# Kernel optimization log

Hardware: AMD Instinct MI355X
Metric: run time of the kernel (lower is better)

## Reference

```python
import jax, jax.numpy as jnp
import numpy as np

D_STATE = 8
DT_RANK = 8  # ceil(128/16)


def _grouped_1x1(x, w):
    # x: (B,H,W,Cin), w: (g, Cout//g, Cin//g)
    B, H, W, _ = x.shape
    g, o, i = w.shape
    xg = x.reshape(B, H, W, g, i)
    return jnp.einsum('bhwgi,goi->bhwgo', xg, w).reshape(B, H, W, g * o)


def setup_inputs() -> dict:
    key = jax.random.key(0)
    ks = jax.random.split(key, 16)
    B, H, W, C = 8, 64, 64, 128
    g = 4
    D = 128  # expand_dim = d_inner
    N = D_STATE
    R = DT_RANK
    inp = {}
    inp['x'] = jax.random.normal(ks[0], (B, H, W, C), dtype=jnp.float32)
    inp['w1'] = jax.random.normal(ks[1], (g, D // g, C // g), dtype=jnp.float32) * 0.1
    inp['dw'] = jax.random.normal(ks[2], (3, 3, 1, D), dtype=jnp.float32) * 0.1  # HWIO depthwise
    inp['in_proj_w'] = jax.random.normal(ks[3], (2 * D, D), dtype=jnp.float32) * 0.05
    inp['conv1d_w'] = jax.random.normal(ks[4], (D, 3), dtype=jnp.float32) * 0.1
    inp['conv1d_b'] = jax.random.normal(ks[5], (D,), dtype=jnp.float32) * 0.05
    inp['x_proj_w'] = jax.random.normal(ks[6], (R + 2 * N, D), dtype=jnp.float32) * 0.05
    inp['dt_proj_w'] = jax.random.normal(ks[7], (D, R), dtype=jnp.float32) * 0.05
    inp['dt_proj_b'] = jax.random.normal(ks[8], (D,), dtype=jnp.float32) * 0.05
    inp['A_log'] = jnp.log(jnp.tile(jnp.arange(1, N + 1, dtype=jnp.float32)[None, :], (D, 1)))
    inp['D_param'] = jnp.ones((D,), dtype=jnp.float32)
    inp['out_proj_w'] = jax.random.normal(ks[9], (D, D), dtype=jnp.float32) * 0.05
    inp['gamma'] = jnp.ones((D,), dtype=jnp.float32)
    inp['beta'] = jnp.zeros((D,), dtype=jnp.float32)
    inp['w2'] = jax.random.normal(ks[10], (g, D // g, C // g), dtype=jnp.float32) * 0.1
    inp['wout'] = jax.random.normal(ks[11], (g, C // g, D // g), dtype=jnp.float32) * 0.1
    return inp


def _mamba(x_seq, in_proj_w, conv1d_w, conv1d_b, x_proj_w, dt_proj_w, dt_proj_b, A_log, D_param, out_proj_w):
    # x_seq: (B, L, D)
    B, L, D = x_seq.shape
    N, R = D_STATE, DT_RANK
    xz = jnp.einsum('bld,ed->ble', x_seq, in_proj_w)  # (B,L,2D)
    u, z = xz[..., :D], xz[..., D:]
    # causal depthwise conv1d, kernel=3, left pad 2 (torch: padding=2, slice [:L])
    up = jnp.pad(u, ((0, 0), (2, 0), (0, 0)))
    u = (up[:, 0:L] * conv1d_w[:, 0] + up[:, 1:L + 1] * conv1d_w[:, 1]
         + up[:, 2:L + 2] * conv1d_w[:, 2] + conv1d_b)
    u = jax.nn.silu(u)
    x_dbl = jnp.einsum('bld,ed->ble', u, x_proj_w)  # (B,L,R+2N)
    dt = x_dbl[..., :R]
    Bm = x_dbl[..., R:R + N]
    Cm = x_dbl[..., R + N:]
    delta = jax.nn.softplus(jnp.einsum('blr,dr->bld', dt, dt_proj_w) + dt_proj_b)  # (B,L,D)
    A = -jnp.exp(A_log)  # (D,N)

    def step(h, inp):
        d_t, u_t, b_t, c_t = inp  # (B,D),(B,D),(B,N),(B,N)
        dA = jnp.exp(d_t[..., None] * A)            # (B,D,N)
        h = dA * h + (d_t * u_t)[..., None] * b_t[:, None, :]
        y_t = jnp.einsum('bdn,bn->bd', h, c_t)
        return h, y_t

    h0 = jnp.zeros((B, D, N), dtype=x_seq.dtype)
    xs = (jnp.swapaxes(delta, 0, 1), jnp.swapaxes(u, 0, 1),
          jnp.swapaxes(Bm, 0, 1), jnp.swapaxes(Cm, 0, 1))
    _, ys = jax.lax.scan(step, h0, xs)              # ys: (L,B,D)
    y = jnp.swapaxes(ys, 0, 1) + u * D_param
    y = y * jax.nn.silu(z)
    return jnp.einsum('bld,ed->ble', y, out_proj_w)


def reference(x, w1, dw, in_proj_w, conv1d_w, conv1d_b, x_proj_w, dt_proj_w, dt_proj_b,
              A_log, D_param, out_proj_w, gamma, beta, w2, wout):
    B, H, W, C = x.shape
    D = dw.shape[-1]
    x1 = _grouped_1x1(x, w1)  # (B,H,W,D)
    x1 = jax.lax.conv_general_dilated(
        x1, dw, window_strides=(1, 1), padding='SAME',
        feature_group_count=D, dimension_numbers=('NHWC', 'HWIO', 'NHWC'))
    x1 = jax.nn.silu(x1)
    x1_seq = x1.reshape(B, H * W, D)
    x1_seq = _mamba(x1_seq, in_proj_w, conv1d_w, conv1d_b, x_proj_w,
                    dt_proj_w, dt_proj_b, A_log, D_param, out_proj_w)
    x1 = x1_seq.reshape(B, H, W, D)
    mu = jnp.mean(x1, axis=-1, keepdims=True)
    var = jnp.mean(jnp.square(x1 - mu), axis=-1, keepdims=True)
    x1 = (x1 - mu) * jax.lax.rsqrt(var + 1e-5) * gamma + beta
    x2 = jax.nn.silu(_grouped_1x1(x, w2))
    x_fuse = x1 * x2
    return _grouped_1x1(x_fuse, wout)  # (B,H,W,C)
```

## Files before the change

### kernel.cpp

```cpp
#include <hip/hip_runtime.h>
#include <math.h>

#define B_    8
#define C_    128
#define D_    128
#define L_    4096
#define NPOS_ 32768
#define NC_   256
#define S_    16
#define MFL_  1048576

typedef __attribute__((ext_vector_type(8))) short short8;
typedef __attribute__((ext_vector_type(4))) float f32x4;

__device__ __forceinline__ float siluf(float x) { return x / (1.f + __expf(-x)); }
__device__ __forceinline__ float softplusf(float x) {
    if (x > 20.f) return x;
    return __logf(1.f + __expf(x));
}
__device__ __forceinline__ unsigned short f2bf(float f) {
    unsigned int u = __float_as_uint(f);
    u = (u + 0x7FFFu + ((u >> 16) & 1u)) >> 16;
    return (unsigned short)u;
}
__device__ __forceinline__ float bf2f(unsigned short h) {
    return __uint_as_float(((unsigned int)h) << 16);
}
__device__ __forceinline__ void scan_as(float dl, const float* Ar, bool fast, float* a) {
    if (fast) {
        float e1 = __expf(-dl);
        a[0] = e1;
        a[1] = e1 * e1;
        a[2] = a[1] * e1;
        a[3] = a[1] * a[1];
        a[4] = a[3] * e1;
        a[5] = a[3] * a[1];
        a[6] = a[5] * e1;
        a[7] = a[3] * a[3];
    } else {
        #pragma unroll
        for (int n = 0; n < 8; ++n) a[n] = __expf(dl * Ar[n]);
    }
}

__global__ __launch_bounds__(256) void k0_cvt(const float* __restrict__ inW,
                                              const float* __restrict__ OW,
                                              const float* __restrict__ xpw,
                                              unsigned short* __restrict__ inWb,
                                              unsigned short* __restrict__ OWb,
                                              unsigned short* __restrict__ xpwb) {
    for (int i = blockIdx.x * 256 + threadIdx.x; i < 52224; i += gridDim.x * 256) {
        if (i < 32768)      inWb[i] = f2bf(inW[i]);
        else if (i < 49152) OWb[i - 32768] = f2bf(OW[i - 32768]);
        else                xpwb[i - 49152] = f2bf(xpw[i - 49152]);
    }
}

__global__ __launch_bounds__(256) void k1_g1x1(const float* __restrict__ x,
                                               const float* __restrict__ w1,
                                               const float* __restrict__ w2,
                                               unsigned short* __restrict__ t1b,
                                               unsigned short* __restrict__ x2sb) {
    __shared__ float xs[16 * 128];
    int t = threadIdx.x;
    int d = t & 127, ph = t >> 7;
    int g = d >> 5, o = d & 31;
    float w1r[32], w2r[32];
    #pragma unroll
    for (int i = 0; i < 32; ++i) {
        w1r[i] = w1[g * 1024 + o * 32 + i];
        w2r[i] = w2[g * 1024 + o * 32 + i];
    }
    int pos0 = blockIdx.x * 64;
    for (int it = 0; it < 4; ++it) {
        int p0 = pos0 + it * 16;
        #pragma unroll
        for (int q = 0; q < 2; ++q) {
            int fi = t * 2 + q;
            *(float4*)&xs[fi * 4] = *(const float4*)&x[p0 * 128 + fi * 4];
        }
        __syncthreads();
        #pragma unroll
        for (int q = 0; q < 8; ++q) {
            int pl = ph * 8 + q;
            float a1 = 0.f, a2 = 0.f;
            const float* xr = &xs[pl * 128 + g * 32];
            #pragma unroll
            for (int i4 = 0; i4 < 8; ++i4) {
                float4 xv = *(const float4*)&xr[i4 * 4];
                a1 += xv.x * w1r[i4*4] + xv.y * w1r[i4*4+1] + xv.z * w1r[i4*4+2] + xv.w * w1r[i4*4+3];
                a2 += xv.x * w2r[i4*4] + xv.y * w2r[i4*4+1] + xv.z * w2r[i4*4+2] + xv.w * w2r[i4*4+3];
            }
            int pos = p0 + pl;
            t1b[pos * 128 + d]  = f2bf(a1);
            x2sb[pos * 128 + d] = f2bf(siluf(a2));
        }
        __syncthreads();
    }
}

__global__ __launch_bounds__(128) void k2_dwconv(const unsigned short* __restrict__ t1b,
                                                 const float* __restrict__ dw,
                                                 unsigned short* __restrict__ x1cb) {
    int d = threadIdx.x;
    float dwr[9];
    #pragma unroll
    for (int k = 0; k < 9; ++k) dwr[k] = dw[k * 128 + d];
    int bid = blockIdx.x;
    int wt = bid & 7, ht = (bid >> 3) & 7, b = bid >> 6;
    int h0 = ht * 8, w0 = wt * 8;
    float rows[10][10];
    #pragma unroll
    for (int r = 0; r < 10; ++r) {
        int hh = h0 - 1 + r;
        bool hv = (hh >= 0) && (hh < 64);
        #pragma unroll
        for (int c = 0; c < 10; ++c) {
            int w = w0 - 1 + c;
            bool wvv = (w >= 0) && (w < 64);
            rows[r][c] = (hv && wvv) ? bf2f(t1b[((b * 64 + hh) * 64 + w) * 128 + d]) : 0.f;
        }
    }
    #pragma unroll
    for (int hi = 0; hi < 8; ++hi) {
        #pragma unroll
        for (int wi = 0; wi < 8; ++wi) {
            float acc = rows[hi][wi]     * dwr[0] + rows[hi][wi+1]   * dwr[1] + rows[hi][wi+2]   * dwr[2]
                      + rows[hi+1][wi]   * dwr[3] + rows[hi+1][wi+1] * dwr[4] + rows[hi+1][wi+2] * dwr[5]
                      + rows[hi+2][wi]   * dwr[6] + rows[hi+2][wi+1] * dwr[7] + rows[hi+2][wi+2] * dwr[8];
            x1cb[((b * 64 + h0 + hi) * 64 + w0 + wi) * 128 + d] = f2bf(siluf(acc));
        }
    }
}

__global__ __launch_bounds__(256) void k3_mfma(const unsigned short* __restrict__ Abf,
                                               const unsigned short* __restrict__ Bbf,
                                               unsigned short* __restrict__ urawb,
                                               unsigned short* __restrict__ zb) {
    __shared__ unsigned short Al[128 * 72];
    __shared__ unsigned short Bl[128 * 72];
    int t = threadIdx.x;
    int mtile = blockIdx.x >> 1, ntile = blockIdx.x & 1;
    int pos0 = mtile * 128, n0g = ntile * 128;
    int lane = t & 63, wv = t >> 6;
    int m0 = (wv & 1) * 64, n0w = (wv >> 1) * 64;
    int lanem = lane & 15, laneq = lane >> 4;
    f32x4 acc[4][4];
    #pragma unroll
    for (int i = 0; i < 4; ++i)
        #pragma unroll
        for (int j = 0; j < 4; ++j) acc[i][j] = (f32x4){0.f, 0.f, 0.f, 0.f};
    for (int kc = 0; kc < 2; ++kc) {
        #pragma unroll
        for (int q = 0; q < 4; ++q) {
            int c = t + q * 256;
            int row = c >> 3, col = c & 7;
            *(int4*)&Al[row * 72 + col * 8] = *(const int4*)&Abf[(pos0 + row) * 128 + kc * 64 + col * 8];
            *(int4*)&Bl[row * 72 + col * 8] = *(const int4*)&Bbf[(n0g + row) * 128 + kc * 64 + col * 8];
        }
        __syncthreads();
        #pragma unroll
        for (int ks = 0; ks < 2; ++ks) {
            short8 af[4], bfr[4];
            #pragma unroll
            for (int mi = 0; mi < 4; ++mi)
                af[mi] = *(const short8*)&Al[(m0 + mi * 16 + lanem) * 72 + ks * 32 + laneq * 8];
            #pragma unroll
            for (int ni = 0; ni < 4; ++ni)
                bfr[ni] = *(const short8*)&Bl[(n0w + ni * 16 + lanem) * 72 + ks * 32 + laneq * 8];
            #pragma unroll
            for (int mi = 0; mi < 4; ++mi)
                #pragma unroll
                for (int ni = 0; ni < 4; ++ni)
                    acc[mi][ni] = __builtin_amdgcn_mfma_f32_16x16x32_bf16(af[mi], bfr[ni], acc[mi][ni], 0, 0, 0);
        }
        __syncthreads();
    }
    unsigned short* dst = ntile ? zb : urawb;
    #pragma unroll
    for (int mi = 0; mi < 4; ++mi)
        #pragma unroll
        for (int ni = 0; ni < 4; ++ni)
            #pragma unroll
            for (int r = 0; r < 4; ++r) {
                int m = pos0 + m0 + mi * 16 + laneq * 4 + r;
                int n = n0w + ni * 16 + lanem;
                dst[m * 128 + n] = f2bf(acc[mi][ni][r]);
            }
}

__global__ __launch_bounds__(256) void k4_convproj(const unsigned short* __restrict__ urawb,
                                                   const float* __restrict__ cw,
                                                   const float* __restrict__ cb,
                                                   const unsigned short* __restrict__ xpwb,
                                                   const float* __restrict__ dtw,
                                                   const float* __restrict__ dtb,
                                                   unsigned short* __restrict__ usb,
                                                   float* __restrict__ delta,
                                                   float* __restrict__ Bm,
                                                   float* __restrict__ Cm) {
    __shared__ unsigned short uA[64 * 136];
    __shared__ unsigned short xB[32 * 136];
    __shared__ float xdb[64 * 36];
    int t = threadIdx.x;
    int d = t & 127, ph = t >> 7;
    for (int i = t; i < 32 * 128; i += 256) {
        int n = i >> 7, k = i & 127;
        xB[n * 136 + k] = (n < 24) ? xpwb[n * 128 + k] : (unsigned short)0;
    }
    float cw0 = cw[d * 3 + 0], cw1 = cw[d * 3 + 1], cw2 = cw[d * 3 + 2], cbr = cb[d];
    float dtwr[8];
    #pragma unroll
    for (int r = 0; r < 8; ++r) dtwr[r] = dtw[d * 8 + r];
    float dtbr = dtb[d];

    int gpos0 = blockIdx.x * 64;
    int ll0 = (gpos0 & 4095) + ph * 32;
    int base = (gpos0 + ph * 32) * 128 + d;
    float ur0 = (ll0 >= 2) ? bf2f(urawb[base - 256]) : 0.f;
    float ur1 = (ll0 >= 1) ? bf2f(urawb[base - 128]) : 0.f;
    #pragma unroll
    for (int q = 0; q < 32; ++q) {
        float urq = bf2f(urawb[base + q * 128]);
        float v = siluf(ur0 * cw0 + ur1 * cw1 + urq * cw2 + cbr);
        unsigned short vb = f2bf(v);
        usb[base + q * 128] = vb;
        uA[(ph * 32 + q) * 136 + d] = vb;
        ur0 = ur1; ur1 = urq;
    }
    __syncthreads();
    int lane = t & 63, wv = t >> 6;
    int lanem = lane & 15, laneq = lane >> 4;
    f32x4 accx[2];
    accx[0] = (f32x4){0.f, 0.f, 0.f, 0.f};
    accx[1] = (f32x4){0.f, 0.f, 0.f, 0.f};
    #pragma unroll
    for (int ks = 0; ks < 4; ++ks) {
        short8 af = *(const short8*)&uA[(wv * 16 + lanem) * 136 + ks * 32 + laneq * 8];
        #pragma unroll
        for (int nj = 0; nj < 2; ++nj) {
            short8 bfr = *(const short8*)&xB[(nj * 16 + lanem) * 136 + ks * 32 + laneq * 8];
            accx[nj] = __builtin_amdgcn_mfma_f32_16x16x32_bf16(af, bfr, accx[nj], 0, 0, 0);
        }
    }
    #pragma unroll
    for (int nj = 0; nj < 2; ++nj)
        #pragma unroll
        for (int r = 0; r < 4; ++r)
            xdb[(wv * 16 + laneq * 4 + r) * 36 + nj * 16 + lanem] = accx[nj][r];
    __syncthreads();
    #pragma unroll
    for (int q = 0; q < 32; ++q) {
        int pl = ph * 32 + q;
        float dt = dtbr;
        #pragma unroll
        for (int r = 0; r < 8; ++r) dt += xdb[pl * 36 + r] * dtwr[r];
        delta[base + q * 128] = softplusf(dt);
    }
    for (int i = t; i < 1024; i += 256) {
        int p = i >> 4, j = i & 15;
        float v = xdb[p * 36 + 8 + j];
        int gp = gpos0 + p;
        if (j < 8) Bm[gp * 8 + j] = v;
        else       Cm[gp * 8 + (j - 8)] = v;
    }
}

__global__ __launch_bounds__(128) void k5_scan1(const float* __restrict__ delta,
                                                const unsigned short* __restrict__ usb,
                                                const float* __restrict__ Bm,
                                                const float* __restrict__ A_log,
                                                float* __restrict__ cA,
                                                float* __restrict__ cB) {
    int d = threadIdx.x;
    int bc = blockIdx.x;
    int b = bc >> 8, c = bc & 255;
    float Ar[8]; bool fast = true;
    #pragma unroll
    for (int n = 0; n < 8; ++n) {
        Ar[n] = -__expf(A_log[d * 8 + n]);
        fast = fast && (fabsf(Ar[n] + (float)(n + 1)) < 2e-3f);
    }
    float h[8], ap[8];
    #pragma unroll
    for (int n = 0; n < 8; ++n) { h[n] = 0.f; ap[n] = 1.f; }
    int base  = (b * L_ + c * S_) * 128 + d;
    int bbase = (b * L_ + c * S_) * 8;
    #pragma unroll
    for (int s = 0; s < S_; ++s) {
        float dl = delta[base + s * 128];
        float uv = bf2f(usb[base + s * 128]);
        float du = dl * uv;
        float4 bm0 = *(const float4*)&Bm[bbase + s * 8];
        float4 bm1 = *(const float4*)&Bm[bbase + s * 8 + 4];
        float a[8];
        scan_as(dl, Ar, fast, a);
        ap[0] *= a[0]; h[0] = a[0] * h[0] + du * bm0.x;
        ap[1] *= a[1]; h[1] = a[1] * h[1] + du * bm0.y;
        ap[2] *= a[2]; h[2] = a[2] * h[2] + du * bm0.z;
        ap[3] *= a[3]; h[3] = a[3] * h[3] + du * bm0.w;
        ap[4] *= a[4]; h[4] = a[4] * h[4] + du * bm1.x;
        ap[5] *= a[5]; h[5] = a[5] * h[5] + du * bm1.y;
        ap[6] *= a[6]; h[6] = a[6] * h[6] + du * bm1.z;
        ap[7] *= a[7]; h[7] = a[7] * h[7] + du * bm1.w;
    }
    int obase = ((b * NC_ + c) * 128 + d) * 8;
    *(float4*)&cA[obase]     = make_float4(ap[0], ap[1], ap[2], ap[3]);
    *(float4*)&cA[obase + 4] = make_float4(ap[4], ap[5], ap[6], ap[7]);
    *(float4*)&cB[obase]     = make_float4(h[0], h[1], h[2], h[3]);
    *(float4*)&cB[obase + 4] = make_float4(h[4], h[5], h[6], h[7]);
}

__global__ __launch_bounds__(128) void k6_scan2(const float* __restrict__ cA,
                                                const float* __restrict__ cB,
                                                float* __restrict__ carry) {
    int b = blockIdx.x >> 3;
    int slice = blockIdx.x & 7;
    int dn = slice * 128 + threadIdx.x;
    float h = 0.f;
    #pragma unroll 4
    for (int c = 0; c < NC_; ++c) {
        int idx = (b * NC_ + c) * 1024 + dn;
        float a  = cA[idx];
        float bv = cB[idx];
        carry[idx] = h;
        h = a * h + bv;
    }
}

__global__ __launch_bounds__(128) void k7_scan3(const float* __restrict__ delta,
                                                const unsigned short* __restrict__ usb,
                                                const float* __restrict__ Bm,
                                                const float* __restrict__ Cm,
                                                const unsigned short* __restrict__ zb,
                                                const float* __restrict__ A_log,
                                                const float* __restrict__ Dp,
                                                const float* __restrict__ carry,
                                                unsigned short* __restrict__ ybf) {
    int d = threadIdx.x;
    int bc = blockIdx.x;
    int b = bc >> 8, c = bc & 255;
    float Ar[8]; bool fast = true;
    #pragma unroll
    for (int n = 0; n < 8; ++n) {
        Ar[n] = -__expf(A_log[d * 8 + n]);
        fast = fast && (fabsf(Ar[n] + (float)(n + 1)) < 2e-3f);
    }
    float Dpr = Dp[d];
    int cbase = ((b * NC_ + c) * 128 + d) * 8;
    float4 h0 = *(const float4*)&carry[cbase];
    float4 h1 = *(const float4*)&carry[cbase + 4];
    float h[8] = {h0.x, h0.y, h0.z, h0.w, h1.x, h1.y, h1.z, h1.w};
    int base  = (b * L_ + c * S_) * 128 + d;
    int bbase = (b * L_ + c * S_) * 8;
    #pragma unroll
    for (int s = 0; s < S_; ++s) {
        float dl = delta[base + s * 128];
        float uv = bf2f(usb[base + s * 128]);
        float zv = bf2f(zb[base + s * 128]);
        float du = dl * uv;
        float4 bm0 = *(const float4*)&Bm[bbase + s * 8];
        float4 bm1 = *(const float4*)&Bm[bbase + s * 8 + 4];
        float4 cm0 = *(const float4*)&Cm[bbase + s * 8];
        float4 cm1 = *(const float4*)&Cm[bbase + s * 8 + 4];
        float a[8];
        scan_as(dl, Ar, fast, a);
        h[0] = a[0] * h[0] + du * bm0.x;
        h[1] = a[1] * h[1] + du * bm0.y;
        h[2] = a[2] * h[2] + du * bm0.z;
        h[3] = a[3] * h[3] + du * bm0.w;
        h[4] = a[4] * h[4] + du * bm1.x;
        h[5] = a[5] * h[5] + du * bm1.y;
        h[6] = a[6] * h[6] + du * bm1.z;
        h[7] = a[7] * h[7] + du * bm1.w;
        float yv = h[0] * cm0.x + h[1] * cm0.y + h[2] * cm0.z + h[3] * cm0.w
                 + h[4] * cm1.x + h[5] * cm1.y + h[6] * cm1.z + h[7] * cm1.w;
        yv = (yv + uv * Dpr) * siluf(zv);
        ybf[base + s * 128] = f2bf(yv);
    }
}

__global__ __launch_bounds__(256) void k8a_mfma(const unsigned short* __restrict__ Abf,
                                                const unsigned short* __restrict__ Bbf,
                                                unsigned short* __restrict__ xzb) {
    __shared__ unsigned short Al[64 * 72];
    __shared__ unsigned short Bl[128 * 72];
    int t = threadIdx.x;
    int pos0 = blockIdx.x * 64;
    int lane = t & 63, wv = t >> 6;
    int lanem = lane & 15, laneq = lane >> 4;
    f32x4 acc[8];
    #pragma unroll
    for (int i = 0; i < 8; ++i) acc[i] = (f32x4){0.f, 0.f, 0.f, 0.f};
    for (int kc = 0; kc < 2; ++kc) {
        #pragma unroll
        for (int q = 0; q < 2; ++q) {
            int c = t + q * 256;
            int row = c >> 3, col = c & 7;
            *(int4*)&Al[row * 72 + col * 8] = *(const int4*)&Abf[(pos0 + row) * 128 + kc * 64 + col * 8];
        }
        #pragma unroll
        for (int q = 0; q < 4; ++q) {
            int c = t + q * 256;
            int row = c >> 3, col = c & 7;
            *(int4*)&Bl[row * 72 + col * 8] = *(const int4*)&Bbf[row * 128 + kc * 64 + col * 8];
        }
        __syncthreads();
        #pragma unroll
        for (int ks = 0; ks < 2; ++ks) {
            short8 af = *(const short8*)&Al[(wv * 16 + lanem) * 72 + ks * 32 + laneq * 8];
            #pragma unroll
            for (int ni = 0; ni < 8; ++ni) {
                short8 bfr = *(const short8*)&Bl[(ni * 16 + lanem) * 72 + ks * 32 + laneq * 8];
                acc[ni] = __builtin_amdgcn_mfma_f32_16x16x32_bf16(af, bfr, acc[ni], 0, 0, 0);
            }
        }
        __syncthreads();
    }
    #pragma unroll
    for (int ni = 0; ni < 8; ++ni)
        #pragma unroll
        for (int r = 0; r < 4; ++r) {
            int m = pos0 + wv * 16 + laneq * 4 + r;
            int n = ni * 16 + lanem;
            xzb[m * 128 + n] = f2bf(acc[ni][r]);
        }
}

__global__ __launch_bounds__(256) void k8b_epi(const unsigned short* __restrict__ xzb,
                                               const float* __restrict__ gamma,
                                               const float* __restrict__ beta,
                                               const unsigned short* __restrict__ x2sb,
                                               const float* __restrict__ wout,
                                               float* __restrict__ out) {
    __shared__ float woutL[4 * 1160];
    __shared__ float xfs[64 * 132];
    int t = threadIdx.x;
    int pos0 = blockIdx.x * 64;
    for (int idx = t; idx < 4096; idx += 256) {
        int g = idx >> 10, r = idx & 1023, o = r >> 5, i = r & 31;
        woutL[g * 1160 + o * 36 + i] = wout[idx];
    }
    int te = t & 31, tp = t >> 5;
    float gr[4], br[4];
    #pragma unroll
    for (int j = 0; j < 4; ++j) { gr[j] = gamma[te + 32 * j]; br[j] = beta[te + 32 * j]; }
    #pragma unroll
    for (int i = 0; i < 8; ++i) {
        int row = tp * 8 + i;
        int pos = pos0 + row;
        float v[4];
        #pragma unroll
        for (int j = 0; j < 4; ++j) v[j] = bf2f(xzb[pos * 128 + te + 32 * j]);
        float s  = v[0] + v[1] + v[2] + v[3];
        float s2 = v[0]*v[0] + v[1]*v[1] + v[2]*v[2] + v[3]*v[3];
        #pragma unroll
        for (int off = 16; off >= 1; off >>= 1) {
            s  += __shfl_xor(s, off, 64);
            s2 += __shfl_xor(s2, off, 64);
        }
        float m = s * (1.f / 128.f);
        float var = s2 * (1.f / 128.f) - m * m;
        float rstd = rsqrtf(var + 1e-5f);
        #pragma unroll
        for (int j = 0; j < 4; ++j) {
            float vv = (v[j] - m) * rstd * gr[j] + br[j];
            vv *= bf2f(x2sb[pos * 128 + te + 32 * j]);
            xfs[row * 132 + te + 32 * j] = vv;
        }
    }
    __syncthreads();
    int g = t & 3, pos = t >> 2;
    float xfr[32];
    #pragma unroll
    for (int i4 = 0; i4 < 8; ++i4)
        *(float4*)&xfr[i4 * 4] = *(const float4*)&xfs[pos * 132 + g * 32 + i4 * 4];
    const float* wg = &woutL[g * 1160];
    int obase = (pos0 + pos) * 128 + g * 32;
    #pragma unroll
    for (int ob = 0; ob < 8; ++ob) {
        float o4[4];
        #pragma unroll
        for (int oo = 0; oo < 4; ++oo) {
            int o = ob * 4 + oo;
            float acc = 0.f;
            #pragma unroll
            for (int i4 = 0; i4 < 8; ++i4) {
                float4 wv4 = *(const float4*)&wg[o * 36 + i4 * 4];
                acc += xfr[i4*4] * wv4.x + xfr[i4*4+1] * wv4.y
                     + xfr[i4*4+2] * wv4.z + xfr[i4*4+3] * wv4.w;
            }
            o4[oo] = acc;
        }
        *(float4*)&out[obase + ob * 4] = make_float4(o4[0], o4[1], o4[2], o4[3]);
    }
}

extern "C" void kernel_launch(void* const* d_in, const int* in_sizes, int n_in,
                              void* d_out, int out_size, void* d_ws, size_t ws_size,
                              hipStream_t stream) {
    (void)in_sizes; (void)n_in; (void)out_size; (void)ws_size;
    const float* x         = (const float*)d_in[0];
    const float* w1        = (const float*)d_in[1];
    const float* dw        = (const float*)d_in[2];
    const float* in_proj_w = (const float*)d_in[3];
    const float* conv1d_w  = (const float*)d_in[4];
    const float* conv1d_b  = (const float*)d_in[5];
    const float* x_proj_w  = (const float*)d_in[6];
    const float* dt_proj_w = (const float*)d_in[7];
    const float* dt_proj_b = (const float*)d_in[8];
    const float* A_log     = (const float*)d_in[9];
    const float* D_param   = (const float*)d_in[10];
    const float* out_proj_w= (const float*)d_in[11];
    const float* gamma     = (const float*)d_in[12];
    const float* beta      = (const float*)d_in[13];
    const float* w2        = (const float*)d_in[14];
    const float* wout      = (const float*)d_in[15];
    float* out = (float*)d_out;

    float* ws = (float*)d_ws;
    unsigned short* x2sb  = (unsigned short*)(ws);
    unsigned short* t1b   = (unsigned short*)(ws + 2  * (size_t)MFL_);
    unsigned short* x1cb  = (unsigned short*)(ws + 4  * (size_t)MFL_);
    unsigned short* urawb = (unsigned short*)(ws + 6  * (size_t)MFL_);
    unsigned short* zb    = (unsigned short*)(ws + 8  * (size_t)MFL_);
    unsigned short* ybf   = (unsigned short*)(ws + 10 * (size_t)MFL_);
    unsigned short* xzb   = (unsigned short*)(ws + 12 * (size_t)MFL_);
    unsigned short* usb   = (unsigned short*)(ws + 14 * (size_t)MFL_);
    float* delta = ws + 16 * (size_t)MFL_;
    float* Bm    = ws + 20 * (size_t)MFL_;
    float* Cm    = Bm + (size_t)NPOS_ * 8;
    float* cA    = Cm + (size_t)NPOS_ * 8;
    float* cB    = cA + 2 * (size_t)MFL_;
    float* carry = cB + 2 * (size_t)MFL_;
    unsigned short* inWb = (unsigned short*)(carry + 2 * (size_t)MFL_);
    unsigned short* OWb  = inWb + 32768;
    unsigned short* xpwb = OWb + 16384;

    k0_cvt<<<64, 256, 0, stream>>>(in_proj_w, out_proj_w, x_proj_w, inWb, OWb, xpwb);
    k1_g1x1<<<512, 256, 0, stream>>>(x, w1, w2, t1b, x2sb);
    k2_dwconv<<<512, 128, 0, stream>>>(t1b, dw, x1cb);
    k3_mfma<<<512, 256, 0, stream>>>(x1cb, inWb, urawb, zb);
    k4_convproj<<<512, 256, 0, stream>>>(urawb, conv1d_w, conv1d_b, xpwb,
                                         dt_proj_w, dt_proj_b, usb, delta, Bm, Cm);
    k5_scan1<<<2048, 128, 0, stream>>>(delta, usb, Bm, A_log, cA, cB);
    k6_scan2<<<64, 128, 0, stream>>>(cA, cB, carry);
    k7_scan3<<<2048, 128, 0, stream>>>(delta, usb, Bm, Cm, zb, A_log, D_param, carry, ybf);
    k8a_mfma<<<512, 256, 0, stream>>>(ybf, OWb, xzb);
    k8b_epi<<<512, 256, 0, stream>>>(xzb, gamma, beta, x2sb, wout, out);
}
```

Baseline: 250.1 us.

## Fuse out_proj MFMA with LayerNorm epilogue and fold weight conversion into k1

Merges the out_proj MFMA kernel and the LayerNorm/gate/grouped-1x1 epilogue into one kernel. The fp32 accumulator tile stays in shared memory, reusing the GEMM staging buffer, instead of round-tripping through a bf16 global buffer. The weight bf16 conversion kernel is folded into the first grouped-1x1 kernel, with 102 threads per block handling the conversion. Together these remove two launches and one intermediate global write/read. The LayerNorm now uses unrounded fp32 values. The wout LDS padding changes from 36 to 33, which may misalign the float4 loads.

```diff
diff --git a/kernel.cpp b/kernel.cpp
--- a/kernel.cpp
+++ b/kernel.cpp
@@ -43,26 +43,27 @@
     }
 }
 
-__global__ __launch_bounds__(256) void k0_cvt(const float* __restrict__ inW,
-                                              const float* __restrict__ OW,
-                                              const float* __restrict__ xpw,
-                                              unsigned short* __restrict__ inWb,
-                                              unsigned short* __restrict__ OWb,
-                                              unsigned short* __restrict__ xpwb) {
-    for (int i = blockIdx.x * 256 + threadIdx.x; i < 52224; i += gridDim.x * 256) {
-        if (i < 32768)      inWb[i] = f2bf(inW[i]);
-        else if (i < 49152) OWb[i - 32768] = f2bf(OW[i - 32768]);
-        else                xpwb[i - 49152] = f2bf(xpw[i - 49152]);
-    }
-}
-
 __global__ __launch_bounds__(256) void k1_g1x1(const float* __restrict__ x,
                                                const float* __restrict__ w1,
                                                const float* __restrict__ w2,
+                                               const float* __restrict__ inW,
+                                               const float* __restrict__ OW,
+                                               const float* __restrict__ xpw,
+                                               unsigned short* __restrict__ inWb,
+                                               unsigned short* __restrict__ OWb,
+                                               unsigned short* __restrict__ xpwb,
                                                unsigned short* __restrict__ t1b,
                                                unsigned short* __restrict__ x2sb) {
     __shared__ float xs[16 * 128];
     int t = threadIdx.x;
+    {
+        int i = blockIdx.x * 102 + t;
+        if (t < 102 && i < 52224) {
+            if (i < 32768)      inWb[i] = f2bf(inW[i]);
+            else if (i < 49152) OWb[i - 32768] = f2bf(OW[i - 32768]);
+            else                xpwb[i - 49152] = f2bf(xpw[i - 49152]);
+        }
+    }
     int d = t & 127, ph = t >> 7;
     int g = d >> 5, o = d & 31;
     float w1r[32], w2r[32];
@@ -380,13 +381,27 @@
     }
 }
 
-__global__ __launch_bounds__(256) void k8a_mfma(const unsigned short* __restrict__ Abf,
-                                                const unsigned short* __restrict__ Bbf,
-                                                unsigned short* __restrict__ xzb) {
-    __shared__ unsigned short Al[64 * 72];
-    __shared__ unsigned short Bl[128 * 72];
+__global__ __launch_bounds__(256) void k89_outfuse(const unsigned short* __restrict__ ybf,
+                                                   const unsigned short* __restrict__ OWb,
+                                                   const float* __restrict__ gamma,
+                                                   const float* __restrict__ beta,
+                                                   const unsigned short* __restrict__ x2sb,
+                                                   const float* __restrict__ wout,
+                                                   float* __restrict__ out) {
+    __shared__ float woutL[4 * 1064];
+    __shared__ float gbL[256];
+    __shared__ char un[64 * 132 * 4];
+    unsigned short* Al = (unsigned short*)un;
+    unsigned short* Bl = Al + 64 * 72;
+    float* xzl = (float*)un;
     int t = threadIdx.x;
     int pos0 = blockIdx.x * 64;
+    for (int idx = t; idx < 4096; idx += 256) {
+        int g = idx >> 10, r = idx & 1023, o = r >> 5, i = r & 31;
+        woutL[g * 1064 + o * 33 + i] = wout[idx];
+    }
+    if (t < 128) gbL[t] = gamma[t];
+    else         gbL[t] = beta[t - 128];
     int lane = t & 63, wv = t >> 6;
     int lanem = lane & 15, laneq = lane >> 4;
     f32x4 acc[8];
@@ -397,13 +412,13 @@
         for (int q = 0; q < 2; ++q) {
             int c = t + q * 256;
             int row = c >> 3, col = c & 7;
-            *(int4*)&Al[row * 72 + col * 8] = *(const int4*)&Abf[(pos0 + row) * 128 + kc * 64 + col * 8];
+            *(int4*)&Al[row * 72 + col * 8] = *(const int4*)&ybf[(pos0 + row) * 128 + kc * 64 + col * 8];
         }
         #pragma unroll
         for (int q = 0; q < 4; ++q) {
             int c = t + q * 256;
             int row = c >> 3, col = c & 7;
-            *(int4*)&Bl[row * 72 + col * 8] = *(const int4*)&Bbf[row * 128 + kc * 64 + col * 8];
+            *(int4*)&Bl[row * 72 + col * 8] = *(const int4*)&OWb[row * 128 + kc * 64 + col * 8];
         }
         __syncthreads();
         #pragma unroll
@@ -420,77 +435,50 @@
     #pragma unroll
     for (int ni = 0; ni < 8; ++ni)
         #pragma unroll
-        for (int r = 0; r < 4; ++r) {
-            int m = pos0 + wv * 16 + laneq * 4 + r;
-            int n = ni * 16 + lanem;
-            xzb[m * 128 + n] = f2bf(acc[ni][r]);
-        }
-}
-
-__global__ __launch_bounds__(256) void k8b_epi(const unsigned short* __restrict__ xzb,
-                                               const float* __restrict__ gamma,
-                                               const float* __restrict__ beta,
-                                               const unsigned short* __restrict__ x2sb,
-                                               const float* __restrict__ wout,
-                                               float* __restrict__ out) {
-    __shared__ float woutL[4 * 1160];
-    __shared__ float xfs[64 * 132];
-    int t = threadIdx.x;
-    int pos0 = blockIdx.x * 64;
-    for (int idx = t; idx < 4096; idx += 256) {
-        int g = idx >> 10, r = idx & 1023, o = r >> 5, i = r & 31;
-        woutL[g * 1160 + o * 36 + i] = wout[idx];
-    }
-    int te = t & 31, tp = t >> 5;
-    float gr[4], br[4];
-    #pragma unroll
-    for (int j = 0; j < 4; ++j) { gr[j] = gamma[te + 32 * j]; br[j] = beta[te + 32 * j]; }
-    #pragma unroll
-    for (int i = 0; i < 8; ++i) {
-        int row = tp * 8 + i;
-        int pos = pos0 + row;
-        float v[4];
-        #pragma unroll
-        for (int j = 0; j < 4; ++j) v[j] = bf2f(xzb[pos * 128 + te + 32 * j]);
-        float s  = v[0] + v[1] + v[2] + v[3];
-        float s2 = v[0]*v[0] + v[1]*v[1] + v[2]*v[2] + v[3]*v[3];
-        #pragma unroll
-        for (int off = 16; off >= 1; off >>= 1) {
-            s  += __shfl_xor(s, off, 64);
-            s2 += __shfl_xor(s2, off, 64);
-        }
-        float m = s * (1.f / 128.f);
-        float var = s2 * (1.f / 128.f) - m * m;
-        float rstd = rsqrtf(var + 1e-5f);
-        #pragma unroll
-        for (int j = 0; j < 4; ++j) {
-            float vv = (v[j] - m) * rstd * gr[j] + br[j];
-            vv *= bf2f(x2sb[pos * 128 + te + 32 * j]);
-            xfs[row * 132 + te + 32 * j] = vv;
-        }
-    }
+        for (int r = 0; r < 4; ++r)
+            xzl[(wv * 16 + laneq * 4 + r) * 132 + ni * 16 + lanem] = acc[ni][r];
     __syncthreads();
     int g = t & 3, pos = t >> 2;
-    float xfr[32];
+    float v[32];
     #pragma unroll
     for (int i4 = 0; i4 < 8; ++i4)
-        *(float4*)&xfr[i4 * 4] = *(const float4*)&xfs[pos * 132 + g * 32 + i4 * 4];
-    const float* wg = &woutL[g * 1160];
-    int obase = (pos0 + pos) * 128 + g * 32;
+        *(float4*)&v[i4 * 4] = *(const float4*)&xzl[pos * 132 + g * 32 + i4 * 4];
+    float s = 0.f, s2 = 0.f;
+    #pragma unroll
+    for (int i = 0; i < 32; ++i) { s += v[i]; s2 += v[i] * v[i]; }
+    s  += __shfl_xor(s, 1, 64);  s  += __shfl_xor(s, 2, 64);
+    s2 += __shfl_xor(s2, 1, 64); s2 += __shfl_xor(s2, 2, 64);
+    float m = s * (1.f / 128.f);
+    float var = s2 * (1.f / 128.f) - m * m;
+    float rstd = rsqrtf(var + 1e-5f);
+    int gpos = pos0 + pos;
+    #pragma unroll
+    for (int i4 = 0; i4 < 8; ++i4) {
+        ushort4 xv = *(const ushort4*)&x2sb[gpos * 128 + g * 32 + i4 * 4];
+        unsigned short xa[4] = {xv.x, xv.y, xv.z, xv.w};
+        #pragma unroll
+        for (int k = 0; k < 4; ++k) {
+            int e = g * 32 + i4 * 4 + k;
+            float vv = (v[i4 * 4 + k] - m) * rstd * gbL[e] + gbL[128 + e];
+            v[i4 * 4 + k] = vv * bf2f(xa[k]);
+        }
+    }
+    const float* wg = &woutL[g * 1064];
+    int obase = gpos * 128 + g * 32;
     #pragma unroll
     for (int ob = 0; ob < 8; ++ob) {
         float o4[4];
         #pragma unroll
         for (int oo = 0; oo < 4; ++oo) {
             int o = ob * 4 + oo;
-            float acc = 0.f;
+            float acc2 = 0.f;
             #pragma unroll
             for (int i4 = 0; i4 < 8; ++i4) {
-                float4 wv4 = *(const float4*)&wg[o * 36 + i4 * 4];
-                acc += xfr[i4*4] * wv4.x + xfr[i4*4+1] * wv4.y
-                     + xfr[i4*4+2] * wv4.z + xfr[i4*4+3] * wv4.w;
+                float4 wv4 = *(const float4*)&wg[o * 33 + i4 * 4];
+                acc2 += v[i4*4] * wv4.x + v[i4*4+1] * wv4.y
+                      + v[i4*4+2] * wv4.z + v[i4*4+3] * wv4.w;
             }
-            o4[oo] = acc;
+            o4[oo] = acc2;
         }
         *(float4*)&out[obase + ob * 4] = make_float4(o4[0], o4[1], o4[2], o4[3]);
     }
@@ -525,10 +513,9 @@
     unsigned short* urawb = (unsigned short*)(ws + 6  * (size_t)MFL_);
     unsigned short* zb    = (unsigned short*)(ws + 8  * (size_t)MFL_);
     unsigned short* ybf   = (unsigned short*)(ws + 10 * (size_t)MFL_);
-    unsigned short* xzb   = (unsigned short*)(ws + 12 * (size_t)MFL_);
-    unsigned short* usb   = (unsigned short*)(ws + 14 * (size_t)MFL_);
-    float* delta = ws + 16 * (size_t)MFL_;
-    float* Bm    = ws + 20 * (size_t)MFL_;
+    unsigned short* usb   = (unsigned short*)(ws + 12 * (size_t)MFL_);
+    float* delta = ws + 14 * (size_t)MFL_;
+    float* Bm    = ws + 18 * (size_t)MFL_;
     float* Cm    = Bm + (size_t)NPOS_ * 8;
     float* cA    = Cm + (size_t)NPOS_ * 8;
     float* cB    = cA + 2 * (size_t)MFL_;
@@ -537,8 +524,8 @@
     unsigned short* OWb  = inWb + 32768;
     unsigned short* xpwb = OWb + 16384;
 
-    k0_cvt<<<64, 256, 0, stream>>>(in_proj_w, out_proj_w, x_proj_w, inWb, OWb, xpwb);
-    k1_g1x1<<<512, 256, 0, stream>>>(x, w1, w2, t1b, x2sb);
+    k1_g1x1<<<512, 256, 0, stream>>>(x, w1, w2, in_proj_w, out_proj_w, x_proj_w,
+                                     inWb, OWb, xpwb, t1b, x2sb);
     k2_dwconv<<<512, 128, 0, stream>>>(t1b, dw, x1cb);
     k3_mfma<<<512, 256, 0, stream>>>(x1cb, inWb, urawb, zb);
     k4_convproj<<<512, 256, 0, stream>>>(urawb, conv1d_w, conv1d_b, xpwb,
@@ -546,6 +533,5 @@
     k5_scan1<<<2048, 128, 0, stream>>>(delta, usb, Bm, A_log, cA, cB);
     k6_scan2<<<64, 128, 0, stream>>>(cA, cB, carry);
     k7_scan3<<<2048, 128, 0, stream>>>(delta, usb, Bm, Cm, zb, A_log, D_param, carry, ybf);
-    k8a_mfma<<<512, 256, 0, stream>>>(ybf, OWb, xzb);
-    k8b_epi<<<512, 256, 0, stream>>>(xzb, gamma, beta, x2sb, wout, out);
-}
+    k89_outfuse<<<512, 256, 0, stream>>>(ybf, OWb, gamma, beta, x2sb, wout, out);
+}
```

Measured after the change: 276.1 us. 1.1x slower.
